# Optimization experiments

Measured on AMD Instinct MI355X. Metric: run time of the kernel, lower is better.

Reference implementation:

```python
import jax, jax.numpy as jnp
import numpy as np

B, L, D, C, NL = 32, 512, 768, 97, 2  # batch, seq_len, hidden, class_nums, gat_layers


def setup_inputs() -> dict:
    key = jax.random.key(0)
    ks = jax.random.split(key, 16)

    def n(k, shape, scale=0.02):
        return jax.random.normal(k, shape, dtype=jnp.float32) * scale

    return dict(
        x=n(ks[0], (B, L, D), 1.0),                 # encoder output
        pos1=jnp.ones((B, L), jnp.float32),          # entity-1 position mask
        pos2=jnp.ones((B, L), jnp.float32),          # entity-2 position mask
        mask=jnp.ones((B, L), jnp.int32),            # attention mask (1 = keep)
        emb=n(ks[1], (C, D), 1.0),                   # relation label embedding table
        rel_w=n(ks[2], (D, D)), rel_b=jnp.zeros((D,), jnp.float32),
        # per-layer, per-RA (axis1: 0=ra1, 1=ra2) parameters
        qw=n(ks[3], (NL, 2, D, D)), qb=jnp.zeros((NL, 2, D), jnp.float32),
        kw=n(ks[4], (NL, 2, D, D)), kb=jnp.zeros((NL, 2, D), jnp.float32),
        vw=n(ks[5], (NL, 2, D, D)), vb=jnp.zeros((NL, 2, D), jnp.float32),
        sw=n(ks[6], (NL, 2, 2 * D)), sb=jnp.zeros((NL, 2), jnp.float32),   # score: Linear(2d,1)
        gw=n(ks[7], (NL, 2, 2 * D)), gb=jnp.zeros((NL, 2), jnp.float32),   # gate:  Linear(2d,1)
        fc1_w=n(ks[8], (3 * D, D)), fc1_b=jnp.zeros((D,), jnp.float32),
        fc2_w=n(ks[9], (D,)), fc2_b=jnp.zeros((), jnp.float32),
    )


def _relation_attention(p, x, qw, qb, kw, kb, vw, vb, sw, sb, gw, gb, mask):
    # p: (b, c, d) queries; x: (b, l, d) keys/values
    d = p.shape[-1]
    q = jnp.einsum('bcd,de->bce', p, qw) + qb          # (b, c, d)
    k = jnp.einsum('bld,de->ble', x, kw) + kb          # (b, l, d)
    # score = Linear(concat([q_i, k_j])) is separable: q@sw[:d] + k@sw[d:] + sb
    score = (q @ sw[:d])[:, :, None] + (k @ sw[d:])[:, None, :] + sb  # (b, c, l)
    if mask is not None:
        score = jnp.where(mask[:, None, :] == 0, jnp.float32(-1e9), score)
    attn = jax.nn.softmax(score, axis=2)
    v = jnp.einsum('bld,de->ble', x, vw) + vb          # (b, l, d)
    out = jnp.einsum('bcl,bld->bcd', attn, v) + p      # (b, c, d)
    # gate = sigmoid(Linear(concat([out, p]))), also separable
    g = jax.nn.sigmoid(out @ gw[:d] + p @ gw[d:] + gb)[..., None]
    return g * out + (1.0 - g) * p


def reference(x, pos1, pos2, mask, emb, rel_w, rel_b,
              qw, qb, kw, kb, vw, vb, sw, sb, gw, gb,
              fc1_w, fc1_b, fc2_w, fc2_b):
    b, d = x.shape[0], x.shape[-1]
    # p = relation(embedding(arange(C))) broadcast over batch
    p = emb @ rel_w + rel_b                            # (C, d)
    p = jnp.broadcast_to(p[None], (b,) + p.shape)      # (b, C, d)

    for li in range(qw.shape[0]):
        x = _relation_attention(x, p, qw[li, 0], qb[li, 0], kw[li, 0], kb[li, 0],
                                vw[li, 0], vb[li, 0], sw[li, 0], sb[li, 0],
                                gw[li, 0], gb[li, 0], None) + x
        p = _relation_attention(p, x, qw[li, 1], qb[li, 1], kw[li, 1], kb[li, 1],
                                vw[li, 1], vb[li, 1], sw[li, 1], sb[li, 1],
                                gw[li, 1], gb[li, 1], mask) + p

    def pool_avg(pos):
        return jnp.sum(x * pos[:, :, None], axis=1) / jnp.sum(pos, axis=1)[:, None]

    e1 = pool_avg(pos1)                                # (b, d)
    e2 = pool_avg(pos2)                                # (b, d)
    cshape = p.shape                                   # (b, C, d)
    pc = jnp.concatenate([p,
                          jnp.broadcast_to(e1[:, None, :], cshape),
                          jnp.broadcast_to(e2[:, None, :], cshape)], axis=2)  # (b, C, 3d)
    h = jnp.tanh(pc @ fc1_w + fc1_b)                   # (b, C, d)
    logits = jax.nn.sigmoid(h @ fc2_w + fc2_b)         # (b, C)
    pred = jnp.argmax(logits, axis=1)                  # (b,)
    return logits, pred
```

## Files before the change

### kernel.cpp

```cpp
#include <hip/hip_runtime.h>
#include <math.h>

#define NBLK 512
#define NTHR 256
static const int Bb = 32, Ls = 512, Dd = 768, Cc = 97;

struct KArgs {
    const float *x0, *pos1, *pos2;
    const int* mask;
    const float *emb, *rel_w, *rel_b, *kw, *vw, *vb, *sw, *gw, *gb;
    const float *fc1w, *fc1b, *fc2w, *fc2b;
    float* out;
    float *p0b, *pp, *sc, *avx1, *avx2, *av1, *av2, *aw1, *aw2, *S0, *S1, *xp1, *xp2, *geb;
    float *kvecs, *pdots, *g1buf, *xd, *gx1, *gx2, *awb;
    float* zbase;
    int zcount;
};

__device__ __forceinline__ float sigm(float x) { return 1.f / (1.f + expf(-x)); }

__device__ __forceinline__ float wred(float v) {
#pragma unroll
    for (int o = 32; o > 0; o >>= 1) v += __shfl_down(v, o, 64);
    return v;
}

__device__ __forceinline__ float blk_sum4(float v, float* shr) {
    v = wred(v);
    int t = threadIdx.x;
    if ((t & 63) == 0) shr[t >> 6] = v;
    __syncthreads();
    float r = shr[0] + shr[1] + shr[2] + shr[3];
    __syncthreads();
    return r;
}

__device__ void sgemm_dev(const float* __restrict__ A, const float* __restrict__ W,
                          const float* __restrict__ bias, float* __restrict__ C,
                          int M, int N, int K, int KC, int bx, int by, int bz,
                          float* As, float* Ws) {
    int tid = threadIdx.x;
    int tx = tid & 15, ty = tid >> 4;
    int bn = bx * 64, bm = by * 64;
    int kb = bz * KC;
    int arow = tid >> 2, akq = (tid & 3) << 2;
    int wrow = tid >> 4, wcol = (tid & 15) << 2;
    int gar = bm + arow;
    bool aval = gar < M;
    const float* Ap = A + (size_t)gar * K + kb + akq;
    const float* Wp = W + (size_t)(kb + wrow) * N + bn + wcol;
    float acc[4][4] = {{0.f}};
    float4 a4 = make_float4(0.f, 0.f, 0.f, 0.f);
    if (aval) a4 = *(const float4*)Ap;
    float4 w4 = *(const float4*)Wp;
    for (int k0 = 0; k0 < KC; k0 += 16) {
        __syncthreads();
        As[(akq + 0) * 64 + arow] = a4.x; As[(akq + 1) * 64 + arow] = a4.y;
        As[(akq + 2) * 64 + arow] = a4.z; As[(akq + 3) * 64 + arow] = a4.w;
        *(float4*)&Ws[wrow * 64 + wcol] = w4;
        __syncthreads();
        if (k0 + 16 < KC) {
            if (aval) a4 = *(const float4*)(Ap + k0 + 16);
            w4 = *(const float4*)(Wp + (size_t)(k0 + 16) * N);
        }
#pragma unroll
        for (int kk = 0; kk < 16; ++kk) {
            float4 a = *(const float4*)&As[kk * 64 + (ty << 2)];
            float4 b = *(const float4*)&Ws[kk * 64 + (tx << 2)];
            acc[0][0]+=a.x*b.x; acc[0][1]+=a.x*b.y; acc[0][2]+=a.x*b.z; acc[0][3]+=a.x*b.w;
            acc[1][0]+=a.y*b.x; acc[1][1]+=a.y*b.y; acc[1][2]+=a.y*b.z; acc[1][3]+=a.y*b.w;
            acc[2][0]+=a.z*b.x; acc[2][1]+=a.z*b.y; acc[2][2]+=a.z*b.z; acc[2][3]+=a.z*b.w;
            acc[3][0]+=a.w*b.x; acc[3][1]+=a.w*b.y; acc[3][2]+=a.w*b.z; acc[3][3]+=a.w*b.w;
        }
    }
    int gc = bn + (tx << 2);
    float4 bz4 = make_float4(0.f, 0.f, 0.f, 0.f);
    if (bz == 0 && bias) bz4 = *(const float4*)(bias + gc);
#pragma unroll
    for (int i = 0; i < 4; ++i) {
        int gr = bm + (ty << 2) + i;
        if (gr < M) {
            float* cp = C + (size_t)gr * N + gc;
            atomicAdd(cp + 0, acc[i][0] + bz4.x); atomicAdd(cp + 1, acc[i][1] + bz4.y);
            atomicAdd(cp + 2, acc[i][2] + bz4.z); atomicAdd(cp + 3, acc[i][3] + bz4.w);
        }
    }
}

__device__ void attn_gemv(const KArgs& a, int phase, int jlin,
                          float* xs, float* lw, float* shr) {
    int t = threadIdx.x;
    int jt = jlin % 3, b = (jlin / 3) % 32, kseg = jlin / 96;
    float v = -3.0e38f, g1 = 0.f;
    if (t < Cc) {
        if (phase == 0) v = a.pdots[t];
        else {
            g1 = sigm(a.pdots[194 + t] + a.sc[128 + b] + a.gb[1]);
            v = 2.f * a.pdots[97 + t] + g1 * a.sc[160 + b];
        }
    }
    if (phase == 1 && jt == 0 && kseg == 0 && t < Cc) a.g1buf[(size_t)b * Cc + t] = g1;
    float m = v;
#pragma unroll
    for (int o = 32; o > 0; o >>= 1) m = fmaxf(m, __shfl_down(m, o, 64));
    if ((t & 63) == 0) shr[t >> 6] = m;
    __syncthreads();
    m = fmaxf(fmaxf(shr[0], shr[1]), fmaxf(shr[2], shr[3]));
    __syncthreads();
    float e = (t < Cc) ? expf(v - m) : 0.f;
    float s = blk_sum4(e, shr);
    float wc = e / s;
    if (t < Cc) lw[t] = wc;
    float cg1 = blk_sum4(wc * g1, shr);
    float alpha = (phase == 0) ? 1.f : 2.f;
    if (t < 96) {
        int d = kseg * 96 + t;
        const float* pc = a.p0b + d;
        float acc2 = 0.f;
#pragma unroll 4
        for (int c = 0; c < Cc; ++c) acc2 += lw[c] * pc[(size_t)c * Dd];
        float val = alpha * acc2;
        if (phase == 1) val += cg1 * a.av1[(size_t)b * Dd + d];
        xs[t] = val;
    }
    __syncthreads();
    const float* W = a.vw + (size_t)(phase == 0 ? 0 : 2) * Dd * Dd;
    const float* bias = a.vb + (phase == 0 ? 0 : 2) * Dd;
    float* outp = (phase == 0) ? a.avx1 : a.avx2;
    int j = jt * 256 + t;
    float acc = (kseg == 0) ? bias[j] : 0.f;
    const float* wp = W + (size_t)(kseg * 96) * Dd + j;
#pragma unroll 8
    for (int dd = 0; dd < 96; ++dd) acc += xs[dd] * wp[(size_t)dd * Dd];
    atomicAdd(&outp[(size_t)b * Dd + j], acc);
    const float* da[4]; const float* db[4]; int nd; float* dout;
    if (phase == 0) {
        da[0]=a.gw;          db[0]=nullptr;
        da[1]=a.kvecs+Dd;    db[1]=nullptr;
        da[2]=a.gw+3072;     db[2]=a.gw+3840;
        da[3]=a.kvecs+3*Dd;  db[3]=nullptr;
        nd = 4; dout = a.sc;
    } else {
        da[0]=a.gw+3072;     db[0]=nullptr;
        da[1]=a.kvecs+3*Dd;  db[1]=nullptr;
        nd = 2; dout = a.sc + 224;
    }
    for (int vv = 0; vv < nd; ++vv) {
        float wv = da[vv][j] + (db[vv] ? db[vv][j] : 0.f);
        float p = blk_sum4(acc * wv, shr);
        if (t == 0) atomicAdd(&dout[vv * 32 + b], p);
    }
}

__device__ void mm_dev(const KArgs& a, int jlin, const float* S, float gamma,
                       const float* avA, const float* coefA, float multA,
                       const float* avB, const float* coefB, float multB,
                       const float* W, const float* bias, float* outp,
                       int ndots, const float* d0a, const float* d0b,
                       const float* d1a, const float* d2a, const float* d2b,
                       float* dout, float* xs, float* shr) {
    int t = threadIdx.x;
    int jt = jlin % 3, b = (jlin / 3) % 32, kseg = jlin / 96;
    if (t < 96) {
        int d = kseg * 96 + t;
        float v = gamma * S[(size_t)b * Dd + d];
        if (avA) v += multA * coefA[b] * avA[(size_t)b * Dd + d];
        if (avB) v += multB * coefB[b] * avB[(size_t)b * Dd + d];
        xs[t] = v;
    }
    __syncthreads();
    int j = jt * 256 + t;
    float acc = (kseg == 0 && bias) ? bias[j] : 0.f;
    const float* wp = W + (size_t)(kseg * 96) * Dd + j;
#pragma unroll 8
    for (int dd = 0; dd < 96; ++dd) acc += xs[dd] * wp[(size_t)dd * Dd];
    atomicAdd(&outp[(size_t)b * Dd + j], acc);
    if (ndots > 0) {
        float wv = d0a[j] + (d0b ? d0b[j] : 0.f);
        float p = blk_sum4(acc * wv, shr);
        if (t == 0) atomicAdd(&dout[b], p);
    }
    if (ndots > 1) {
        float p = blk_sum4(acc * d1a[j], shr);
        if (t == 0) atomicAdd(&dout[32 + b], p);
    }
    if (ndots > 2) {
        float wv = d2a[j] + (d2b ? d2b[j] : 0.f);
        float p = blk_sum4(acc * wv, shr);
        if (t == 0) atomicAdd(&dout[64 + b], p);
    }
}

__device__ void ge_dev(const KArgs& a, int jlin, float* xs, float* xs2) {
    int t = threadIdx.x;
    int jt = jlin % 3, b = (jlin / 3) % 32, kseg = jlin / 96;
    if (t < 96) {
        int d = kseg * 96 + t;
        float a1 = a.avx1[(size_t)b * Dd + d], a2 = a.avx2[(size_t)b * Dd + d];
        xs[t]  = (4.f * a.xp1[(size_t)b * Dd + d] + 2.f * a.sc[448 + b] * a1 + a.sc[480 + b] * a2) * a.sc[576 + b];
        xs2[t] = (4.f * a.xp2[(size_t)b * Dd + d] + 2.f * a.sc[512 + b] * a1 + a.sc[544 + b] * a2) * a.sc[608 + b];
    }
    __syncthreads();
    int j = jt * 256 + t;
    float a1 = 0.f, a2 = 0.f;
    const float* w1 = a.fc1w + (size_t)(Dd + kseg * 96) * Dd + j;
    const float* w2 = a.fc1w + (size_t)(2 * Dd + kseg * 96) * Dd + j;
#pragma unroll 8
    for (int dd = 0; dd < 96; ++dd) {
        a1 += xs[dd] * w1[(size_t)dd * Dd];
        a2 += xs2[dd] * w2[(size_t)dd * Dd];
    }
    float res = a1 + a2 + (kseg == 0 ? a.fc1b[j] : 0.f);
    atomicAdd(&a.geb[(size_t)b * Dd + j], res);
}

__device__ void aw_dual_dev(const KArgs& a, int jlin, float* xs, float* xs2) {
    int t = threadIdx.x;
    int jt = jlin % 3, b = (jlin / 3) % 32, kseg = jlin / 96;
    if (t < 96) {
        int d = kseg * 96 + t;
        xs[t]  = a.av1[(size_t)b * Dd + d];
        xs2[t] = a.av2[(size_t)b * Dd + d];
    }
    __syncthreads();
    int j = jt * 256 + t;
    float a1 = 0.f, a2 = 0.f;
    const float* wp = a.fc1w + (size_t)(kseg * 96) * Dd + j;
#pragma unroll 8
    for (int dd = 0; dd < 96; ++dd) {
        float w = wp[(size_t)dd * Dd];
        a1 += xs[dd] * w;
        a2 += xs2[dd] * w;
    }
    atomicAdd(&a.aw1[(size_t)b * Dd + j], a1);
    atomicAdd(&a.aw2[(size_t)b * Dd + j], a2);
}

__device__ void softgate_dev(const KArgs& a, int phase, int b, float* shr) {
    int t = threadIdx.x;
    float ks[2], ga[2] = {0.f, 0.f}, gb2[2] = {0.f, 0.f};
#pragma unroll
    for (int i = 0; i < 2; ++i) {
        int l = t + (i << 8);
        size_t r = (size_t)b * Ls + l;
        float4 x = *(const float4*)(a.xd + r * 4);
        if (phase == 0) {
            float g = sigm(x.x + a.sc[b] + a.gb[0]);
            a.gx1[r] = g;
            ga[i] = g;
            ks[i] = 2.f * x.y + g * a.sc[32 + b];
        } else {
            float gp = a.gx1[r];
            float g = sigm(2.f * x.z + gp * a.sc[64 + b] + a.sc[224 + b] + a.gb[2]);
            a.gx2[r] = g;
            ga[i] = gp; gb2[i] = g;
            ks[i] = 4.f * x.w + 2.f * gp * a.sc[96 + b] + g * a.sc[256 + b];
        }
        if (a.mask[r] == 0) ks[i] = -1e9f;
    }
    float mx = fmaxf(ks[0], ks[1]);
#pragma unroll
    for (int o = 32; o > 0; o >>= 1) mx = fmaxf(mx, __shfl_down(mx, o, 64));
    if ((t & 63) == 0) shr[t >> 6] = mx;
    __syncthreads();
    mx = fmaxf(fmaxf(shr[0], shr[1]), fmaxf(shr[2], shr[3]));
    __syncthreads();
    float e0 = expf(ks[0] - mx), e1 = expf(ks[1] - mx);
    float s = blk_sum4(e0 + e1, shr);
    float inv = 1.f / s;
    float w0 = e0 * inv, w1 = e1 * inv;
    a.awb[(size_t)b * Ls + t] = w0;
    a.awb[(size_t)b * Ls + t + 256] = w1;
    float ca = blk_sum4(w0 * ga[0] + w1 * ga[1], shr);
    if (phase == 0) {
        if (t == 0) a.sc[320 + b] = ca;
    } else {
        if (t == 0) a.sc[352 + b] = ca;
        float cb = blk_sum4(w0 * gb2[0] + w1 * gb2[1], shr);
        if (t == 0) a.sc[384 + b] = cb;
        float q1a = a.pos1[(size_t)b * Ls + t], q1b = a.pos1[(size_t)b * Ls + t + 256];
        float q2a = a.pos2[(size_t)b * Ls + t], q2b = a.pos2[(size_t)b * Ls + t + 256];
        float s1 = blk_sum4(q1a + q1b, shr);
        float s2 = blk_sum4(q2a + q2b, shr);
        float c11 = blk_sum4(q1a * ga[0] + q1b * ga[1], shr);
        float c12 = blk_sum4(q1a * gb2[0] + q1b * gb2[1], shr);
        float c21 = blk_sum4(q2a * ga[0] + q2b * ga[1], shr);
        float c22 = blk_sum4(q2a * gb2[0] + q2b * gb2[1], shr);
        if (t == 0) {
            a.sc[448 + b] = c11; a.sc[480 + b] = c12;
            a.sc[512 + b] = c21; a.sc[544 + b] = c22;
            a.sc[576 + b] = 1.f / s1; a.sc[608 + b] = 1.f / s2;
        }
    }
}

__device__ void passX_dev(const KArgs& a, int blk, float* S, bool dopos) {
    int t = threadIdx.x;
    if (t >= 192) return;
    int b = blk >> 4, seg = blk & 15, l0 = seg * 32;
    int d4 = t << 2;
    const float* xb = a.x0 + ((size_t)b * Ls + l0) * Dd + d4;
    const float* wb = a.awb + (size_t)b * Ls + l0;
    float4 as = make_float4(0.f,0.f,0.f,0.f);
    float4 a1 = make_float4(0.f,0.f,0.f,0.f);
    float4 a2 = make_float4(0.f,0.f,0.f,0.f);
    for (int l = 0; l < 32; ++l) {
        float4 xv = *(const float4*)(xb + (size_t)l * Dd);
        float wv = wb[l];
        as.x += wv*xv.x; as.y += wv*xv.y; as.z += wv*xv.z; as.w += wv*xv.w;
        if (dopos) {
            float q1 = a.pos1[(size_t)b * Ls + l0 + l], q2 = a.pos2[(size_t)b * Ls + l0 + l];
            a1.x += q1*xv.x; a1.y += q1*xv.y; a1.z += q1*xv.z; a1.w += q1*xv.w;
            a2.x += q2*xv.x; a2.y += q2*xv.y; a2.z += q2*xv.z; a2.w += q2*xv.w;
        }
    }
    float* ds = S + (size_t)b * Dd + d4;
    atomicAdd(ds+0, as.x); atomicAdd(ds+1, as.y); atomicAdd(ds+2, as.z); atomicAdd(ds+3, as.w);
    if (dopos) {
        float* d1 = a.xp1 + (size_t)b * Dd + d4;
        float* d2 = a.xp2 + (size_t)b * Dd + d4;
        atomicAdd(d1+0, a1.x); atomicAdd(d1+1, a1.y); atomicAdd(d1+2, a1.z); atomicAdd(d1+3, a1.w);
        atomicAdd(d2+0, a2.x); atomicAdd(d2+1, a2.y); atomicAdd(d2+2, a2.z); atomicAdd(d2+3, a2.w);
    }
}

__global__ __launch_bounds__(NTHR) void k_zero_kvec(KArgs a) {
    int blk = blockIdx.x, t = threadIdx.x;
    int wv_ = t >> 6, lane = t & 63;
    for (size_t i = (size_t)blk * NTHR + t; i < (size_t)a.zcount; i += (size_t)NBLK * NTHR)
        a.zbase[i] = 0.f;
    int g = blk * 4 + wv_;
    for (int rep = 0; rep < 2; ++rep) {
        int dot = g + rep * 2048;
        if (dot < 3072) {
            int idx = dot / Dd, d = dot - idx * Dd;
            const float* row = a.kw + ((size_t)idx * Dd + d) * Dd;
            const float* swk = a.sw + (size_t)idx * 2 * Dd + Dd;
            float sA = 0.f;
            for (int j = lane; j < Dd; j += 64) sA += row[j] * swk[j];
            sA = wred(sA);
            if (lane == 0) a.kvecs[dot] = sA;
        }
    }
}

__global__ __launch_bounds__(NTHR) void k_gemm1(KArgs a) {
    __shared__ float As[1024], Ws[1024];
    int blk = blockIdx.x;
    sgemm_dev(a.emb, a.rel_w, a.rel_b, a.p0b, Cc, Dd, Dd, 96,
              blk % 12, (blk / 12) % 2, blk / 24, As, Ws);
}

__global__ __launch_bounds__(NTHR) void k_prep2(KArgs a) {
    __shared__ float As[1024], Ws[1024];
    int blk = blockIdx.x, t = threadIdx.x;
    int wv_ = t >> 6, lane = t & 63;
    if (blk < 96) {
        sgemm_dev(a.p0b, a.fc1w, nullptr, a.pp, Cc, Dd, Dd, 192,
                  blk % 12, (blk / 12) % 2, blk / 24, As, Ws);
    } else if (blk < 128) {
        int g2 = (blk - 96) * 4 + wv_;
        for (int k = 0; k < 4; ++k) {
            int j = g2 + k * 128;
            if (k == 3) { if (g2 >= 4) break; j = 384 + g2; }
            if (j >= 388) continue;
            int vv = j / Cc, r = j - vv * Cc;
            const float* va; const float* vb2 = nullptr;
            if (vv == 0) va = a.kvecs;
            else if (vv == 1) va = a.kvecs + 2 * Dd;
            else if (vv == 2) { va = a.gw + 1536; vb2 = a.gw + 2304; }
            else { va = a.gw + 4608; vb2 = a.gw + 5376; }
            const float* row = a.p0b + (size_t)r * Dd;
            float sA = 0.f;
            for (int jj = lane; jj < Dd; jj += 64)
                sA += row[jj] * (va[jj] + (vb2 ? vb2[jj] : 0.f));
            sA = wred(sA);
            if (lane == 0) a.pdots[j] = sA;
        }
    } else {
        float4 gs0[3], k1r[3], gs2[3], k3r[3];
#pragma unroll
        for (int k = 0; k < 3; ++k) {
            int d = (lane << 2) + k * 256;
            float4 ga = *(const float4*)(a.gw + d);
            float4 gbv = *(const float4*)(a.gw + 768 + d);
            gs0[k] = make_float4(ga.x+gbv.x, ga.y+gbv.y, ga.z+gbv.z, ga.w+gbv.w);
            k1r[k] = *(const float4*)(a.kvecs + 768 + d);
            float4 g2a = *(const float4*)(a.gw + 3072 + d);
            float4 g2b = *(const float4*)(a.gw + 3840 + d);
            gs2[k] = make_float4(g2a.x+g2b.x, g2a.y+g2b.y, g2a.z+g2b.z, g2a.w+g2b.w);
            k3r[k] = *(const float4*)(a.kvecs + 2304 + d);
        }
        int gwv = (blk - 128) * 4 + wv_;
        for (int r = gwv; r < Bb * Ls; r += 1536) {
            const float* xr = a.x0 + (size_t)r * Dd;
            float s0 = 0.f, s1 = 0.f, s2 = 0.f, s3 = 0.f;
#pragma unroll
            for (int k = 0; k < 3; ++k) {
                float4 xv = *(const float4*)(xr + (lane << 2) + k * 256);
                s0 += xv.x*gs0[k].x + xv.y*gs0[k].y + xv.z*gs0[k].z + xv.w*gs0[k].w;
                s1 += xv.x*k1r[k].x + xv.y*k1r[k].y + xv.z*k1r[k].z + xv.w*k1r[k].w;
                s2 += xv.x*gs2[k].x + xv.y*gs2[k].y + xv.z*gs2[k].z + xv.w*gs2[k].w;
                s3 += xv.x*k3r[k].x + xv.y*k3r[k].y + xv.z*k3r[k].z + xv.w*k3r[k].w;
            }
            s0 = wred(s0); s1 = wred(s1); s2 = wred(s2); s3 = wred(s3);
            if (lane == 0) {
                float4 o4 = make_float4(s0, s1, s2, s3);
                *(float4*)(a.xd + (size_t)r * 4) = o4;
            }
        }
    }
}

__global__ __launch_bounds__(NTHR) void k_attn(KArgs a, int phase) {
    __shared__ float xs[96], lw[128], shr[16];
    attn_gemv(a, phase, blockIdx.x, xs, lw, shr);
}

__global__ __launch_bounds__(NTHR) void k_softgate(KArgs a, int phase) {
    __shared__ float shr[16];
    softgate_dev(a, phase, blockIdx.x, shr);
}

__global__ __launch_bounds__(NTHR) void k_passX0(KArgs a) {
    passX_dev(a, blockIdx.x, a.S0, true);
}

__global__ __launch_bounds__(NTHR) void k_mm0(KArgs a) {
    __shared__ float xs[96], shr[16];
    mm_dev(a, blockIdx.x, a.S0, 2.f, a.avx1, a.sc + 320, 1.f, nullptr, nullptr, 0.f,
           a.vw + (size_t)1 * Dd * Dd, a.vb + Dd, a.av1,
           3, a.gw + 1536, nullptr, a.kvecs + 2 * Dd, a.gw + 4608, a.gw + 5376,
           a.sc + 128, xs, shr);
}

__global__ __launch_bounds__(NTHR) void k_passX1ge(KArgs a) {
    __shared__ float xs[96], xs2[96];
    int blk = blockIdx.x;
    if (blk < 512) passX_dev(a, blk, a.S1, false);
    else ge_dev(a, blk - 512, xs, xs2);
}

__global__ __launch_bounds__(NTHR) void k_mm1(KArgs a) {
    __shared__ float xs[96], shr[16];
    mm_dev(a, blockIdx.x, a.S1, 4.f, a.avx1, a.sc + 352, 2.f, a.avx2, a.sc + 384, 1.f,
           a.vw + (size_t)3 * Dd * Dd, a.vb + 3 * Dd, a.av2,
           1, a.gw + 4608, nullptr, nullptr, nullptr, nullptr,
           a.sc + 288, xs, shr);
}

__global__ __launch_bounds__(NTHR) void k_awdual(KArgs a) {
    __shared__ float xs[96], xs2[96];
    aw_dual_dev(a, blockIdx.x, xs, xs2);
}

__global__ __launch_bounds__(NTHR) void k_logits(KArgs a) {
    __shared__ float shr[16];
    int blk = blockIdx.x, t = threadIdx.x;
    for (int r = blk; r < Bb * Cc; r += NBLK) {
        int b = r / Cc, c = r - b * Cc;
        float g1 = a.g1buf[r];
        float g2 = sigm(2.f * a.pdots[291 + c] + g1 * a.sc[192 + b] + a.sc[288 + b] + a.gb[3]);
        float ssum = 0.f;
#pragma unroll
        for (int sseg = 0; sseg < 3; ++sseg) {
            int d = t + sseg * 256;
            float h = tanhf(4.f * a.pp[(size_t)c * Dd + d]
                          + 2.f * g1 * a.aw1[(size_t)b * Dd + d]
                          + g2 * a.aw2[(size_t)b * Dd + d]
                          + a.geb[(size_t)b * Dd + d]);
            ssum += h * a.fc2w[d];
        }
        float tt = blk_sum4(ssum, shr);
        if (t == 0) a.out[r] = sigm(tt + a.fc2b[0]);
    }
}

__global__ void k_argmax(KArgs a) {
    int t = threadIdx.x;
    if (t < Bb) {
        const float* row = a.out + (size_t)t * Cc;
        float best = row[0];
        int bi = 0;
        for (int c = 1; c < Cc; ++c) {
            float v = row[c];
            if (v > best) { best = v; bi = c; }
        }
        a.out[Bb * Cc + t] = (float)bi;
    }
}

extern "C" void kernel_launch(void* const* d_in, const int* in_sizes, int n_in,
                              void* d_out, int out_size, void* d_ws, size_t ws_size,
                              hipStream_t stream) {
    KArgs ka;
    ka.x0    = (const float*)d_in[0];
    ka.pos1  = (const float*)d_in[1];
    ka.pos2  = (const float*)d_in[2];
    ka.mask  = (const int*)d_in[3];
    ka.emb   = (const float*)d_in[4];
    ka.rel_w = (const float*)d_in[5];
    ka.rel_b = (const float*)d_in[6];
    ka.kw    = (const float*)d_in[9];
    ka.vw    = (const float*)d_in[11];
    ka.vb    = (const float*)d_in[12];
    ka.sw    = (const float*)d_in[13];
    ka.gw    = (const float*)d_in[15];
    ka.gb    = (const float*)d_in[16];
    ka.fc1w  = (const float*)d_in[17];
    ka.fc1b  = (const float*)d_in[18];
    ka.fc2w  = (const float*)d_in[19];
    ka.fc2b  = (const float*)d_in[20];
    ka.out   = (float*)d_out;

    float* ws = (float*)d_ws;
    size_t off = 0;
    const size_t PD = (size_t)Cc * Dd;
    const size_t BD = (size_t)Bb * Dd;
    ka.p0b  = ws + off; off += PD;
    ka.pp   = ws + off; off += PD;
    ka.sc   = ws + off; off += 640;
    ka.avx1 = ws + off; off += BD;
    ka.avx2 = ws + off; off += BD;
    ka.av1  = ws + off; off += BD;
    ka.av2  = ws + off; off += BD;
    ka.aw1  = ws + off; off += BD;
    ka.aw2  = ws + off; off += BD;
    ka.S0   = ws + off; off += BD;
    ka.S1   = ws + off; off += BD;
    ka.xp1  = ws + off; off += BD;
    ka.xp2  = ws + off; off += BD;
    ka.geb  = ws + off; off += BD;
    ka.zbase = ws;
    ka.zcount = (int)off;
    ka.kvecs = ws + off; off += (size_t)4 * Dd;
    ka.pdots = ws + off; off += 388;
    ka.g1buf = ws + off; off += (size_t)Bb * Cc;
    ka.xd    = ws + off; off += (size_t)Bb * Ls * 4;
    ka.gx1   = ws + off; off += (size_t)Bb * Ls;
    ka.gx2   = ws + off; off += (size_t)Bb * Ls;
    ka.awb   = ws + off; off += (size_t)Bb * Ls;

    k_zero_kvec<<<NBLK, NTHR, 0, stream>>>(ka);
    k_gemm1<<<192, NTHR, 0, stream>>>(ka);
    k_prep2<<<NBLK, NTHR, 0, stream>>>(ka);
    k_attn<<<768, NTHR, 0, stream>>>(ka, 0);
    k_softgate<<<32, NTHR, 0, stream>>>(ka, 0);
    k_passX0<<<NBLK, NTHR, 0, stream>>>(ka);
    k_mm0<<<768, NTHR, 0, stream>>>(ka);
    k_attn<<<768, NTHR, 0, stream>>>(ka, 1);
    k_softgate<<<32, NTHR, 0, stream>>>(ka, 1);
    k_passX1ge<<<1280, NTHR, 0, stream>>>(ka);
    k_mm1<<<768, NTHR, 0, stream>>>(ka);
    k_awdual<<<768, NTHR, 0, stream>>>(ka);
    k_logits<<<NBLK, NTHR, 0, stream>>>(ka);
    k_argmax<<<1, 64, 0, stream>>>(ka);
}
```

Baseline: 339.1 us.

## Merge launch stages, recompute softmax weights per block, drop split-K atomics in pp GEMM

```diff
diff --git a/kernel.cpp b/kernel.cpp
--- a/kernel.cpp
+++ b/kernel.cpp
@@ -12,7 +12,7 @@
     const float *fc1w, *fc1b, *fc2w, *fc2b;
     float* out;
     float *p0b, *pp, *sc, *avx1, *avx2, *av1, *av2, *aw1, *aw2, *S0, *S1, *xp1, *xp2, *geb;
-    float *kvecs, *pdots, *g1buf, *xd, *gx1, *gx2, *awb;
+    float *kvecs, *pdots, *g1buf, *xd;
     float* zbase;
     int zcount;
 };
@@ -35,31 +35,30 @@
     return r;
 }
 
-__device__ void sgemm_dev(const float* __restrict__ A, const float* __restrict__ W,
-                          const float* __restrict__ bias, float* __restrict__ C,
-                          int M, int N, int K, int KC, int bx, int by, int bz,
-                          float* As, float* Ws) {
+__device__ void sgemm_direct(const float* __restrict__ A, const float* __restrict__ W,
+                             const float* __restrict__ bias, float* __restrict__ C,
+                             int M, int N, int K, int bx, int by,
+                             float* As, float* Ws) {
     int tid = threadIdx.x;
     int tx = tid & 15, ty = tid >> 4;
     int bn = bx * 64, bm = by * 64;
-    int kb = bz * KC;
     int arow = tid >> 2, akq = (tid & 3) << 2;
     int wrow = tid >> 4, wcol = (tid & 15) << 2;
     int gar = bm + arow;
     bool aval = gar < M;
-    const float* Ap = A + (size_t)gar * K + kb + akq;
-    const float* Wp = W + (size_t)(kb + wrow) * N + bn + wcol;
+    const float* Ap = A + (size_t)gar * K + akq;
+    const float* Wp = W + (size_t)wrow * N + bn + wcol;
     float acc[4][4] = {{0.f}};
     float4 a4 = make_float4(0.f, 0.f, 0.f, 0.f);
     if (aval) a4 = *(const float4*)Ap;
     float4 w4 = *(const float4*)Wp;
-    for (int k0 = 0; k0 < KC; k0 += 16) {
+    for (int k0 = 0; k0 < K; k0 += 16) {
         __syncthreads();
         As[(akq + 0) * 64 + arow] = a4.x; As[(akq + 1) * 64 + arow] = a4.y;
         As[(akq + 2) * 64 + arow] = a4.z; As[(akq + 3) * 64 + arow] = a4.w;
         *(float4*)&Ws[wrow * 64 + wcol] = w4;
         __syncthreads();
-        if (k0 + 16 < KC) {
+        if (k0 + 16 < K) {
             if (aval) a4 = *(const float4*)(Ap + k0 + 16);
             w4 = *(const float4*)(Wp + (size_t)(k0 + 16) * N);
         }
@@ -75,15 +74,81 @@
     }
     int gc = bn + (tx << 2);
     float4 bz4 = make_float4(0.f, 0.f, 0.f, 0.f);
-    if (bz == 0 && bias) bz4 = *(const float4*)(bias + gc);
+    if (bias) bz4 = *(const float4*)(bias + gc);
 #pragma unroll
     for (int i = 0; i < 4; ++i) {
         int gr = bm + (ty << 2) + i;
         if (gr < M) {
-            float* cp = C + (size_t)gr * N + gc;
-            atomicAdd(cp + 0, acc[i][0] + bz4.x); atomicAdd(cp + 1, acc[i][1] + bz4.y);
-            atomicAdd(cp + 2, acc[i][2] + bz4.z); atomicAdd(cp + 3, acc[i][3] + bz4.w);
-        }
+            float4 o = make_float4(acc[i][0] + bz4.x, acc[i][1] + bz4.y,
+                                   acc[i][2] + bz4.z, acc[i][3] + bz4.w);
+            *(float4*)(C + (size_t)gr * N + gc) = o;
+        }
+    }
+}
+
+__device__ void sm_w(const KArgs& a, int phase, int b, float* shr,
+                     float& w0o, float& w1o, float& ga0, float& ga1,
+                     float& gb0o, float& gb1o) {
+    int t = threadIdx.x;
+    float ks[2], ga[2], gb2[2] = {0.f, 0.f};
+#pragma unroll
+    for (int i = 0; i < 2; ++i) {
+        int l = t + (i << 8);
+        size_t r = (size_t)b * Ls + l;
+        const float* px = a.xd + r * 4;
+        float gp = sigm(px[0] + a.sc[b] + a.gb[0]);
+        if (phase == 0) {
+            ga[i] = gp;
+            ks[i] = 2.f * px[1] + gp * a.sc[32 + b];
+        } else {
+            float g = sigm(2.f * px[2] + gp * a.sc[64 + b] + a.sc[224 + b] + a.gb[2]);
+            ga[i] = gp; gb2[i] = g;
+            ks[i] = 4.f * px[3] + 2.f * gp * a.sc[96 + b] + g * a.sc[256 + b];
+        }
+        if (a.mask[r] == 0) ks[i] = -1e9f;
+    }
+    float mx = fmaxf(ks[0], ks[1]);
+#pragma unroll
+    for (int o = 32; o > 0; o >>= 1) mx = fmaxf(mx, __shfl_down(mx, o, 64));
+    if ((t & 63) == 0) shr[t >> 6] = mx;
+    __syncthreads();
+    mx = fmaxf(fmaxf(shr[0], shr[1]), fmaxf(shr[2], shr[3]));
+    __syncthreads();
+    float e0 = expf(ks[0] - mx), e1 = expf(ks[1] - mx);
+    float s = blk_sum4(e0 + e1, shr);
+    float inv = 1.f / s;
+    w0o = e0 * inv; w1o = e1 * inv;
+    ga0 = ga[0]; ga1 = ga[1];
+    gb0o = gb2[0]; gb1o = gb2[1];
+}
+
+__device__ void coeff0_dev(const KArgs& a, int b, float* shr) {
+    float w0, w1, ga0, ga1, u0, u1;
+    sm_w(a, 0, b, shr, w0, w1, ga0, ga1, u0, u1);
+    float ca = blk_sum4(w0 * ga0 + w1 * ga1, shr);
+    if (threadIdx.x == 0) a.sc[320 + b] = ca;
+}
+
+__device__ void coeff1_dev(const KArgs& a, int b, float* shr) {
+    int t = threadIdx.x;
+    float w0, w1, ga0, ga1, g0, g1;
+    sm_w(a, 1, b, shr, w0, w1, ga0, ga1, g0, g1);
+    float ca = blk_sum4(w0 * ga0 + w1 * ga1, shr);
+    if (t == 0) a.sc[352 + b] = ca;
+    float cb = blk_sum4(w0 * g0 + w1 * g1, shr);
+    if (t == 0) a.sc[384 + b] = cb;
+    float q1a = a.pos1[(size_t)b * Ls + t], q1b = a.pos1[(size_t)b * Ls + t + 256];
+    float q2a = a.pos2[(size_t)b * Ls + t], q2b = a.pos2[(size_t)b * Ls + t + 256];
+    float s1 = blk_sum4(q1a + q1b, shr);
+    float s2 = blk_sum4(q2a + q2b, shr);
+    float c11 = blk_sum4(q1a * ga0 + q1b * ga1, shr);
+    float c12 = blk_sum4(q1a * g0 + q1b * g1, shr);
+    float c21 = blk_sum4(q2a * ga0 + q2b * ga1, shr);
+    float c22 = blk_sum4(q2a * g0 + q2b * g1, shr);
+    if (t == 0) {
+        a.sc[448 + b] = c11; a.sc[480 + b] = c12;
+        a.sc[512 + b] = c21; a.sc[544 + b] = c22;
+        a.sc[576 + b] = 1.f / s1; a.sc[608 + b] = 1.f / s2;
     }
 }
 
@@ -150,6 +215,7 @@
         float p = blk_sum4(acc * wv, shr);
         if (t == 0) atomicAdd(&dout[vv * 32 + b], p);
     }
+    __syncthreads();
 }
 
 __device__ void mm_dev(const KArgs& a, int jlin, const float* S, float gamma,
@@ -197,8 +263,10 @@
     if (t < 96) {
         int d = kseg * 96 + t;
         float a1 = a.avx1[(size_t)b * Dd + d], a2 = a.avx2[(size_t)b * Dd + d];
-        xs[t]  = (4.f * a.xp1[(size_t)b * Dd + d] + 2.f * a.sc[448 + b] * a1 + a.sc[480 + b] * a2) * a.sc[576 + b];
-        xs2[t] = (4.f * a.xp2[(size_t)b * Dd + d] + 2.f * a.sc[512 + b] * a1 + a.sc[544 + b] * a2) * a.sc[608 + b];
+        xs[t]  = (4.f * a.xp1[(size_t)b * Dd + d] + 2.f * a.sc[448 + b] * a1
+                  + a.sc[480 + b] * a2) * a.sc[576 + b];
+        xs2[t] = (4.f * a.xp2[(size_t)b * Dd + d] + 2.f * a.sc[512 + b] * a1
+                  + a.sc[544 + b] * a2) * a.sc[608 + b];
     }
     __syncthreads();
     int j = jt * 256 + t;
@@ -214,216 +282,176 @@
     atomicAdd(&a.geb[(size_t)b * Dd + j], res);
 }
 
-__device__ void aw_dual_dev(const KArgs& a, int jlin, float* xs, float* xs2) {
+__device__ void aw_one(const KArgs& a, int jlin, const float* av, float* outp, float* xs) {
     int t = threadIdx.x;
     int jt = jlin % 3, b = (jlin / 3) % 32, kseg = jlin / 96;
-    if (t < 96) {
-        int d = kseg * 96 + t;
-        xs[t]  = a.av1[(size_t)b * Dd + d];
-        xs2[t] = a.av2[(size_t)b * Dd + d];
-    }
+    if (t < 96) xs[t] = av[(size_t)b * Dd + kseg * 96 + t];
     __syncthreads();
     int j = jt * 256 + t;
-    float a1 = 0.f, a2 = 0.f;
+    float acc = 0.f;
     const float* wp = a.fc1w + (size_t)(kseg * 96) * Dd + j;
 #pragma unroll 8
-    for (int dd = 0; dd < 96; ++dd) {
-        float w = wp[(size_t)dd * Dd];
-        a1 += xs[dd] * w;
-        a2 += xs2[dd] * w;
-    }
-    atomicAdd(&a.aw1[(size_t)b * Dd + j], a1);
-    atomicAdd(&a.aw2[(size_t)b * Dd + j], a2);
-}
-
-__device__ void softgate_dev(const KArgs& a, int phase, int b, float* shr) {
-    int t = threadIdx.x;
-    float ks[2], ga[2] = {0.f, 0.f}, gb2[2] = {0.f, 0.f};
-#pragma unroll
-    for (int i = 0; i < 2; ++i) {
-        int l = t + (i << 8);
-        size_t r = (size_t)b * Ls + l;
-        float4 x = *(const float4*)(a.xd + r * 4);
-        if (phase == 0) {
-            float g = sigm(x.x + a.sc[b] + a.gb[0]);
-            a.gx1[r] = g;
-            ga[i] = g;
-            ks[i] = 2.f * x.y + g * a.sc[32 + b];
-        } else {
-            float gp = a.gx1[r];
-            float g = sigm(2.f * x.z + gp * a.sc[64 + b] + a.sc[224 + b] + a.gb[2]);
-            a.gx2[r] = g;
-            ga[i] = gp; gb2[i] = g;
-            ks[i] = 4.f * x.w + 2.f * gp * a.sc[96 + b] + g * a.sc[256 + b];
-        }
-        if (a.mask[r] == 0) ks[i] = -1e9f;
-    }
-    float mx = fmaxf(ks[0], ks[1]);
-#pragma unroll
-    for (int o = 32; o > 0; o >>= 1) mx = fmaxf(mx, __shfl_down(mx, o, 64));
-    if ((t & 63) == 0) shr[t >> 6] = mx;
-    __syncthreads();
-    mx = fmaxf(fmaxf(shr[0], shr[1]), fmaxf(shr[2], shr[3]));
-    __syncthreads();
-    float e0 = expf(ks[0] - mx), e1 = expf(ks[1] - mx);
-    float s = blk_sum4(e0 + e1, shr);
-    float inv = 1.f / s;
-    float w0 = e0 * inv, w1 = e1 * inv;
-    a.awb[(size_t)b * Ls + t] = w0;
-    a.awb[(size_t)b * Ls + t + 256] = w1;
-    float ca = blk_sum4(w0 * ga[0] + w1 * ga[1], shr);
-    if (phase == 0) {
-        if (t == 0) a.sc[320 + b] = ca;
-    } else {
-        if (t == 0) a.sc[352 + b] = ca;
-        float cb = blk_sum4(w0 * gb2[0] + w1 * gb2[1], shr);
-        if (t == 0) a.sc[384 + b] = cb;
-        float q1a = a.pos1[(size_t)b * Ls + t], q1b = a.pos1[(size_t)b * Ls + t + 256];
-        float q2a = a.pos2[(size_t)b * Ls + t], q2b = a.pos2[(size_t)b * Ls + t + 256];
-        float s1 = blk_sum4(q1a + q1b, shr);
-        float s2 = blk_sum4(q2a + q2b, shr);
-        float c11 = blk_sum4(q1a * ga[0] + q1b * ga[1], shr);
-        float c12 = blk_sum4(q1a * gb2[0] + q1b * gb2[1], shr);
-        float c21 = blk_sum4(q2a * ga[0] + q2b * ga[1], shr);
-        float c22 = blk_sum4(q2a * gb2[0] + q2b * gb2[1], shr);
-        if (t == 0) {
-            a.sc[448 + b] = c11; a.sc[480 + b] = c12;
-            a.sc[512 + b] = c21; a.sc[544 + b] = c22;
-            a.sc[576 + b] = 1.f / s1; a.sc[608 + b] = 1.f / s2;
-        }
-    }
-}
-
-__device__ void passX_dev(const KArgs& a, int blk, float* S, bool dopos) {
-    int t = threadIdx.x;
-    if (t >= 192) return;
+    for (int dd = 0; dd < 96; ++dd) acc += xs[dd] * wp[(size_t)dd * Dd];
+    atomicAdd(&outp[(size_t)b * Dd + j], acc);
+}
+
+__device__ void passX_dev(const KArgs& a, int phase, int blk, float* S, bool dopos,
+                          float* smw, float* shr) {
+    int t = threadIdx.x;
     int b = blk >> 4, seg = blk & 15, l0 = seg * 32;
-    int d4 = t << 2;
-    const float* xb = a.x0 + ((size_t)b * Ls + l0) * Dd + d4;
-    const float* wb = a.awb + (size_t)b * Ls + l0;
-    float4 as = make_float4(0.f,0.f,0.f,0.f);
-    float4 a1 = make_float4(0.f,0.f,0.f,0.f);
-    float4 a2 = make_float4(0.f,0.f,0.f,0.f);
-    for (int l = 0; l < 32; ++l) {
-        float4 xv = *(const float4*)(xb + (size_t)l * Dd);
-        float wv = wb[l];
-        as.x += wv*xv.x; as.y += wv*xv.y; as.z += wv*xv.z; as.w += wv*xv.w;
+    {
+        float w0, w1, u0, u1, u2, u3;
+        sm_w(a, phase, b, shr, w0, w1, u0, u1, u2, u3);
+        smw[t] = w0; smw[t + 256] = w1;
+    }
+    __syncthreads();
+    if (t < 192) {
+        int d4 = t << 2;
+        const float* xb = a.x0 + ((size_t)b * Ls + l0) * Dd + d4;
+        float4 as = make_float4(0.f,0.f,0.f,0.f);
+        float4 a1 = make_float4(0.f,0.f,0.f,0.f);
+        float4 a2 = make_float4(0.f,0.f,0.f,0.f);
+        for (int l = 0; l < 32; ++l) {
+            float4 xv = *(const float4*)(xb + (size_t)l * Dd);
+            float wv = smw[l0 + l];
+            as.x += wv*xv.x; as.y += wv*xv.y; as.z += wv*xv.z; as.w += wv*xv.w;
+            if (dopos) {
+                float q1 = a.pos1[(size_t)b * Ls + l0 + l], q2 = a.pos2[(size_t)b * Ls + l0 + l];
+                a1.x += q1*xv.x; a1.y += q1*xv.y; a1.z += q1*xv.z; a1.w += q1*xv.w;
+                a2.x += q2*xv.x; a2.y += q2*xv.y; a2.z += q2*xv.z; a2.w += q2*xv.w;
+            }
+        }
+        float* ds = S + (size_t)b * Dd + d4;
+        atomicAdd(ds+0, as.x); atomicAdd(ds+1, as.y); atomicAdd(ds+2, as.z); atomicAdd(ds+3, as.w);
         if (dopos) {
-            float q1 = a.pos1[(size_t)b * Ls + l0 + l], q2 = a.pos2[(size_t)b * Ls + l0 + l];
-            a1.x += q1*xv.x; a1.y += q1*xv.y; a1.z += q1*xv.z; a1.w += q1*xv.w;
-            a2.x += q2*xv.x; a2.y += q2*xv.y; a2.z += q2*xv.z; a2.w += q2*xv.w;
-        }
-    }
-    float* ds = S + (size_t)b * Dd + d4;
-    atomicAdd(ds+0, as.x); atomicAdd(ds+1, as.y); atomicAdd(ds+2, as.z); atomicAdd(ds+3, as.w);
-    if (dopos) {
-        float* d1 = a.xp1 + (size_t)b * Dd + d4;
-        float* d2 = a.xp2 + (size_t)b * Dd + d4;
-        atomicAdd(d1+0, a1.x); atomicAdd(d1+1, a1.y); atomicAdd(d1+2, a1.z); atomicAdd(d1+3, a1.w);
-        atomicAdd(d2+0, a2.x); atomicAdd(d2+1, a2.y); atomicAdd(d2+2, a2.z); atomicAdd(d2+3, a2.w);
-    }
-}
-
-__global__ __launch_bounds__(NTHR) void k_zero_kvec(KArgs a) {
+            float* d1 = a.xp1 + (size_t)b * Dd + d4;
+            float* d2 = a.xp2 + (size_t)b * Dd + d4;
+            atomicAdd(d1+0, a1.x); atomicAdd(d1+1, a1.y); atomicAdd(d1+2, a1.z); atomicAdd(d1+3, a1.w);
+            atomicAdd(d2+0, a2.x); atomicAdd(d2+1, a2.y); atomicAdd(d2+2, a2.z); atomicAdd(d2+3, a2.w);
+        }
+    }
+}
+
+__device__ void kvec_dot(const KArgs& a, int dot, int lane) {
+    int idx = dot / Dd, d = dot - idx * Dd;
+    const float* row = a.kw + ((size_t)idx * Dd + d) * Dd;
+    const float* swk = a.sw + (size_t)idx * 2 * Dd + Dd;
+    float sA = 0.f;
+    for (int j = lane; j < Dd; j += 64) sA += row[j] * swk[j];
+    sA = wred(sA);
+    if (lane == 0) a.kvecs[dot] = sA;
+}
+
+__device__ void xdots_dev(const KArgs& a, int r0, int rstep, int lane) {
+    float4 gs0[3], k1r[3], gs2[3], k3r[3];
+#pragma unroll
+    for (int k = 0; k < 3; ++k) {
+        int d = (lane << 2) + k * 256;
+        float4 ga = *(const float4*)(a.gw + d);
+        float4 gbv = *(const float4*)(a.gw + 768 + d);
+        gs0[k] = make_float4(ga.x+gbv.x, ga.y+gbv.y, ga.z+gbv.z, ga.w+gbv.w);
+        k1r[k] = *(const float4*)(a.kvecs + 768 + d);
+        float4 g2a = *(const float4*)(a.gw + 3072 + d);
+        float4 g2b = *(const float4*)(a.gw + 3840 + d);
+        gs2[k] = make_float4(g2a.x+g2b.x, g2a.y+g2b.y, g2a.z+g2b.z, g2a.w+g2b.w);
+        k3r[k] = *(const float4*)(a.kvecs + 2304 + d);
+    }
+    for (int r = r0; r < Bb * Ls; r += rstep) {
+        const float* xr = a.x0 + (size_t)r * Dd;
+        float s0 = 0.f, s1 = 0.f, s2 = 0.f, s3 = 0.f;
+#pragma unroll
+        for (int k = 0; k < 3; ++k) {
+            float4 xv = *(const float4*)(xr + (lane << 2) + k * 256);
+            s0 += xv.x*gs0[k].x + xv.y*gs0[k].y + xv.z*gs0[k].z + xv.w*gs0[k].w;
+            s1 += xv.x*k1r[k].x + xv.y*k1r[k].y + xv.z*k1r[k].z + xv.w*k1r[k].w;
+            s2 += xv.x*gs2[k].x + xv.y*gs2[k].y + xv.z*gs2[k].z + xv.w*gs2[k].w;
+            s3 += xv.x*k3r[k].x + xv.y*k3r[k].y + xv.z*k3r[k].z + xv.w*k3r[k].w;
+        }
+        s0 = wred(s0); s1 = wred(s1); s2 = wred(s2); s3 = wred(s3);
+        if (lane == 0) {
+            float4 o4 = make_float4(s0, s1, s2, s3);
+            *(float4*)(a.xd + (size_t)r * 4) = o4;
+        }
+    }
+}
+
+__device__ void pdots_dev(const KArgs& a, int g2, int lane) {
+    for (int k = 0; k < 4; ++k) {
+        int j = g2 + k * 128;
+        if (k == 3) { if (g2 >= 4) break; j = 384 + g2; }
+        if (j >= 388) continue;
+        int vv = j / Cc, r = j - vv * Cc;
+        const float* va; const float* vb2 = nullptr;
+        if (vv == 0) va = a.kvecs;
+        else if (vv == 1) va = a.kvecs + 2 * Dd;
+        else if (vv == 2) { va = a.gw + 1536; vb2 = a.gw + 2304; }
+        else { va = a.gw + 4608; vb2 = a.gw + 5376; }
+        const float* row = a.p0b + (size_t)r * Dd;
+        float sA = 0.f;
+        for (int jj = lane; jj < Dd; jj += 64)
+            sA += row[jj] * (va[jj] + (vb2 ? vb2[jj] : 0.f));
+        sA = wred(sA);
+        if (lane == 0) a.pdots[j] = sA;
+    }
+}
+
+__device__ void logits_dev(const KArgs& a, int r, float* shr) {
+    int t = threadIdx.x;
+    int b = r / Cc, c = r - b * Cc;
+    float g1 = a.g1buf[r];
+    float g2 = sigm(2.f * a.pdots[291 + c] + g1 * a.sc[192 + b] + a.sc[288 + b] + a.gb[3]);
+    float ssum = 0.f;
+#pragma unroll
+    for (int sseg = 0; sseg < 3; ++sseg) {
+        int d = t + sseg * 256;
+        float h = tanhf(4.f * a.pp[(size_t)c * Dd + d]
+                      + 2.f * g1 * a.aw1[(size_t)b * Dd + d]
+                      + g2 * a.aw2[(size_t)b * Dd + d]
+                      + a.geb[(size_t)b * Dd + d]);
+        ssum += h * a.fc2w[d];
+    }
+    float tt = blk_sum4(ssum, shr);
+    if (t == 0) a.out[r] = sigm(tt + a.fc2b[0]);
+}
+
+__global__ __launch_bounds__(NTHR) void k_zg(KArgs a) {
+    __shared__ float As[1024], Ws[1024];
     int blk = blockIdx.x, t = threadIdx.x;
     int wv_ = t >> 6, lane = t & 63;
-    for (size_t i = (size_t)blk * NTHR + t; i < (size_t)a.zcount; i += (size_t)NBLK * NTHR)
-        a.zbase[i] = 0.f;
-    int g = blk * 4 + wv_;
-    for (int rep = 0; rep < 2; ++rep) {
-        int dot = g + rep * 2048;
-        if (dot < 3072) {
-            int idx = dot / Dd, d = dot - idx * Dd;
-            const float* row = a.kw + ((size_t)idx * Dd + d) * Dd;
-            const float* swk = a.sw + (size_t)idx * 2 * Dd + Dd;
-            float sA = 0.f;
-            for (int j = lane; j < Dd; j += 64) sA += row[j] * swk[j];
-            sA = wred(sA);
-            if (lane == 0) a.kvecs[dot] = sA;
-        }
-    }
-}
-
-__global__ __launch_bounds__(NTHR) void k_gemm1(KArgs a) {
-    __shared__ float As[1024], Ws[1024];
-    int blk = blockIdx.x;
-    sgemm_dev(a.emb, a.rel_w, a.rel_b, a.p0b, Cc, Dd, Dd, 96,
-              blk % 12, (blk / 12) % 2, blk / 24, As, Ws);
+    if (blk < 24) {
+        sgemm_direct(a.emb, a.rel_w, a.rel_b, a.p0b, Cc, Dd, Dd, blk % 12, blk / 12, As, Ws);
+    } else {
+        for (size_t i = (size_t)(blk - 24) * NTHR + t; i < (size_t)a.zcount;
+             i += (size_t)(NBLK - 24) * NTHR)
+            a.zbase[i] = 0.f;
+        for (int dot = (blk - 24) * 4 + wv_; dot < 3072; dot += (NBLK - 24) * 4)
+            kvec_dot(a, dot, lane);
+    }
 }
 
 __global__ __launch_bounds__(NTHR) void k_prep2(KArgs a) {
     __shared__ float As[1024], Ws[1024];
     int blk = blockIdx.x, t = threadIdx.x;
     int wv_ = t >> 6, lane = t & 63;
-    if (blk < 96) {
-        sgemm_dev(a.p0b, a.fc1w, nullptr, a.pp, Cc, Dd, Dd, 192,
-                  blk % 12, (blk / 12) % 2, blk / 24, As, Ws);
-    } else if (blk < 128) {
-        int g2 = (blk - 96) * 4 + wv_;
-        for (int k = 0; k < 4; ++k) {
-            int j = g2 + k * 128;
-            if (k == 3) { if (g2 >= 4) break; j = 384 + g2; }
-            if (j >= 388) continue;
-            int vv = j / Cc, r = j - vv * Cc;
-            const float* va; const float* vb2 = nullptr;
-            if (vv == 0) va = a.kvecs;
-            else if (vv == 1) va = a.kvecs + 2 * Dd;
-            else if (vv == 2) { va = a.gw + 1536; vb2 = a.gw + 2304; }
-            else { va = a.gw + 4608; vb2 = a.gw + 5376; }
-            const float* row = a.p0b + (size_t)r * Dd;
-            float sA = 0.f;
-            for (int jj = lane; jj < Dd; jj += 64)
-                sA += row[jj] * (va[jj] + (vb2 ? vb2[jj] : 0.f));
-            sA = wred(sA);
-            if (lane == 0) a.pdots[j] = sA;
-        }
+    if (blk < 24) {
+        sgemm_direct(a.p0b, a.fc1w, nullptr, a.pp, Cc, Dd, Dd, blk % 12, blk / 12, As, Ws);
+    } else if (blk < 56) {
+        pdots_dev(a, (blk - 24) * 4 + wv_, lane);
     } else {
-        float4 gs0[3], k1r[3], gs2[3], k3r[3];
-#pragma unroll
-        for (int k = 0; k < 3; ++k) {
-            int d = (lane << 2) + k * 256;
-            float4 ga = *(const float4*)(a.gw + d);
-            float4 gbv = *(const float4*)(a.gw + 768 + d);
-            gs0[k] = make_float4(ga.x+gbv.x, ga.y+gbv.y, ga.z+gbv.z, ga.w+gbv.w);
-            k1r[k] = *(const float4*)(a.kvecs + 768 + d);
-            float4 g2a = *(const float4*)(a.gw + 3072 + d);
-            float4 g2b = *(const float4*)(a.gw + 3840 + d);
-            gs2[k] = make_float4(g2a.x+g2b.x, g2a.y+g2b.y, g2a.z+g2b.z, g2a.w+g2b.w);
-            k3r[k] = *(const float4*)(a.kvecs + 2304 + d);
-        }
-        int gwv = (blk - 128) * 4 + wv_;
-        for (int r = gwv; r < Bb * Ls; r += 1536) {
-            const float* xr = a.x0 + (size_t)r * Dd;
-            float s0 = 0.f, s1 = 0.f, s2 = 0.f, s3 = 0.f;
-#pragma unroll
-            for (int k = 0; k < 3; ++k) {
-                float4 xv = *(const float4*)(xr + (lane << 2) + k * 256);
-                s0 += xv.x*gs0[k].x + xv.y*gs0[k].y + xv.z*gs0[k].z + xv.w*gs0[k].w;
-                s1 += xv.x*k1r[k].x + xv.y*k1r[k].y + xv.z*k1r[k].z + xv.w*k1r[k].w;
-                s2 += xv.x*gs2[k].x + xv.y*gs2[k].y + xv.z*gs2[k].z + xv.w*gs2[k].w;
-                s3 += xv.x*k3r[k].x + xv.y*k3r[k].y + xv.z*k3r[k].z + xv.w*k3r[k].w;
-            }
-            s0 = wred(s0); s1 = wred(s1); s2 = wred(s2); s3 = wred(s3);
-            if (lane == 0) {
-                float4 o4 = make_float4(s0, s1, s2, s3);
-                *(float4*)(a.xd + (size_t)r * 4) = o4;
-            }
-        }
-    }
-}
-
-__global__ __launch_bounds__(NTHR) void k_attn(KArgs a, int phase) {
+        xdots_dev(a, (blk - 56) * 4 + wv_, (NBLK - 56) * 4, lane);
+    }
+}
+
+__global__ __launch_bounds__(NTHR) void k_attn0(KArgs a) {
     __shared__ float xs[96], lw[128], shr[16];
-    attn_gemv(a, phase, blockIdx.x, xs, lw, shr);
-}
-
-__global__ __launch_bounds__(NTHR) void k_softgate(KArgs a, int phase) {
-    __shared__ float shr[16];
-    softgate_dev(a, phase, blockIdx.x, shr);
-}
-
-__global__ __launch_bounds__(NTHR) void k_passX0(KArgs a) {
-    passX_dev(a, blockIdx.x, a.S0, true);
+    attn_gemv(a, 0, blockIdx.x, xs, lw, shr);
+}
+
+__global__ __launch_bounds__(NTHR) void k_p3(KArgs a) {
+    __shared__ float smw[512], shr[16];
+    int blk = blockIdx.x;
+    if (blk < 512) passX_dev(a, 0, blk, a.S0, true, smw, shr);
+    else coeff0_dev(a, blk - 512, shr);
 }
 
 __global__ __launch_bounds__(NTHR) void k_mm0(KArgs a) {
@@ -434,46 +462,39 @@
            a.sc + 128, xs, shr);
 }
 
-__global__ __launch_bounds__(NTHR) void k_passX1ge(KArgs a) {
-    __shared__ float xs[96], xs2[96];
+__global__ __launch_bounds__(NTHR) void k_p5(KArgs a) {
+    __shared__ float xs[96], lw[128], shr[16];
     int blk = blockIdx.x;
-    if (blk < 512) passX_dev(a, blk, a.S1, false);
-    else ge_dev(a, blk - 512, xs, xs2);
-}
-
-__global__ __launch_bounds__(NTHR) void k_mm1(KArgs a) {
-    __shared__ float xs[96], shr[16];
-    mm_dev(a, blockIdx.x, a.S1, 4.f, a.avx1, a.sc + 352, 2.f, a.avx2, a.sc + 384, 1.f,
-           a.vw + (size_t)3 * Dd * Dd, a.vb + 3 * Dd, a.av2,
-           1, a.gw + 4608, nullptr, nullptr, nullptr, nullptr,
-           a.sc + 288, xs, shr);
-}
-
-__global__ __launch_bounds__(NTHR) void k_awdual(KArgs a) {
-    __shared__ float xs[96], xs2[96];
-    aw_dual_dev(a, blockIdx.x, xs, xs2);
+    if (blk < 768) attn_gemv(a, 1, blk, xs, lw, shr);
+    else aw_one(a, blk - 768, a.av1, a.aw1, xs);
+}
+
+__global__ __launch_bounds__(NTHR) void k_p6(KArgs a) {
+    __shared__ float smw[512], shr[16];
+    int blk = blockIdx.x;
+    if (blk < 512) passX_dev(a, 1, blk, a.S1, false, smw, shr);
+    else coeff1_dev(a, blk - 512, shr);
+}
+
+__global__ __launch_bounds__(NTHR) void k_p7(KArgs a) {
+    __shared__ float xs[96], xs2[96], shr[16];
+    int blk = blockIdx.x;
+    if (blk < 768)
+        mm_dev(a, blk, a.S1, 4.f, a.avx1, a.sc + 352, 2.f, a.avx2, a.sc + 384, 1.f,
+               a.vw + (size_t)3 * Dd * Dd, a.vb + 3 * Dd, a.av2,
+               1, a.gw + 4608, nullptr, nullptr, nullptr, nullptr,
+               a.sc + 288, xs, shr);
+    else ge_dev(a, blk - 768, xs, xs2);
+}
+
+__global__ __launch_bounds__(NTHR) void k_aw2(KArgs a) {
+    __shared__ float xs[96];
+    aw_one(a, blockIdx.x, a.av2, a.aw2, xs);
 }
 
 __global__ __launch_bounds__(NTHR) void k_logits(KArgs a) {
     __shared__ float shr[16];
-    int blk = blockIdx.x, t = threadIdx.x;
-    for (int r = blk; r < Bb * Cc; r += NBLK) {
-        int b = r / Cc, c = r - b * Cc;
-        float g1 = a.g1buf[r];
-        float g2 = sigm(2.f * a.pdots[291 + c] + g1 * a.sc[192 + b] + a.sc[288 + b] + a.gb[3]);
-        float ssum = 0.f;
-#pragma unroll
-        for (int sseg = 0; sseg < 3; ++sseg) {
-            int d = t + sseg * 256;
-            float h = tanhf(4.f * a.pp[(size_t)c * Dd + d]
-                          + 2.f * g1 * a.aw1[(size_t)b * Dd + d]
-                          + g2 * a.aw2[(size_t)b * Dd + d]
-                          + a.geb[(size_t)b * Dd + d]);
-            ssum += h * a.fc2w[d];
-        }
-        float tt = blk_sum4(ssum, shr);
-        if (t == 0) a.out[r] = sigm(tt + a.fc2b[0]);
-    }
+    for (int r = blockIdx.x; r < Bb * Cc; r += NBLK) logits_dev(a, r, shr);
 }
 
 __global__ void k_argmax(KArgs a) {
@@ -519,6 +540,7 @@
     const size_t BD = (size_t)Bb * Dd;
     ka.p0b  = ws + off; off += PD;
     ka.pp   = ws + off; off += PD;
+    size_t zstart = off;
     ka.sc   = ws + off; off += 640;
     ka.avx1 = ws + off; off += BD;
     ka.avx2 = ws + off; off += BD;
@@ -531,28 +553,22 @@
     ka.xp1  = ws + off; off += BD;
     ka.xp2  = ws + off; off += BD;
     ka.geb  = ws + off; off += BD;
-    ka.zbase = ws;
-    ka.zcount = (int)off;
+    ka.zbase = ws + zstart;
+    ka.zcount = (int)(off - zstart);
     ka.kvecs = ws + off; off += (size_t)4 * Dd;
     ka.pdots = ws + off; off += 388;
     ka.g1buf = ws + off; off += (size_t)Bb * Cc;
     ka.xd    = ws + off; off += (size_t)Bb * Ls * 4;
-    ka.gx1   = ws + off; off += (size_t)Bb * Ls;
-    ka.gx2   = ws + off; off += (size_t)Bb * Ls;
-    ka.awb   = ws + off; off += (size_t)Bb * Ls;
-
-    k_zero_kvec<<<NBLK, NTHR, 0, stream>>>(ka);
-    k_gemm1<<<192, NTHR, 0, stream>>>(ka);
+
+    k_zg<<<NBLK, NTHR, 0, stream>>>(ka);
     k_prep2<<<NBLK, NTHR, 0, stream>>>(ka);
-    k_attn<<<768, NTHR, 0, stream>>>(ka, 0);
-    k_softgate<<<32, NTHR, 0, stream>>>(ka, 0);
-    k_passX0<<<NBLK, NTHR, 0, stream>>>(ka);
+    k_attn0<<<768, NTHR, 0, stream>>>(ka);
+    k_p3<<<544, NTHR, 0, stream>>>(ka);
     k_mm0<<<768, NTHR, 0, stream>>>(ka);
-    k_attn<<<768, NTHR, 0, stream>>>(ka, 1);
-    k_softgate<<<32, NTHR, 0, stream>>>(ka, 1);
-    k_passX1ge<<<1280, NTHR, 0, stream>>>(ka);
-    k_mm1<<<768, NTHR, 0, stream>>>(ka);
-    k_awdual<<<768, NTHR, 0, stream>>>(ka);
+    k_p5<<<1536, NTHR, 0, stream>>>(ka);
+    k_p6<<<544, NTHR, 0, stream>>>(ka);
+    k_p7<<<1536, NTHR, 0, stream>>>(ka);
+    k_aw2<<<768, NTHR, 0, stream>>>(ka);
     k_logits<<<NBLK, NTHR, 0, stream>>>(ka);
     k_argmax<<<1, 64, 0, stream>>>(ka);
 }
```

Measured after the change: 366.5 us. 1.08x slower.
